# Performance work log

Hardware: AMD Instinct MI355X
Metric: run time of the kernel (lower is better)

## Reference

```python
import jax, jax.numpy as jnp
import numpy as np

D_MODEL = 768
N_CH = 2
D_STATE = 16
RANK = 8
LORA_SCALE = 2.0  # alpha/rank = (rank*2.0)/rank
N_LOOPS = 4       # MAX_INFER_LOOPS
BATCH = 1
SEQ = 1024
EPS = 1e-6        # RMSNorm eps


def setup_inputs() -> dict:
    key = jax.random.key(0)
    ks = jax.random.split(key, 12)
    f32 = jnp.float32
    n = lambda k, shp, s: jax.random.normal(k, shp, dtype=f32) * s
    return {
        "x": jax.random.normal(ks[0], (BATCH, SEQ, D_MODEL), dtype=f32),
        "in_proj_base": n(ks[1], (N_CH * D_MODEL, D_MODEL), 0.02),
        "lora_A": n(ks[2], (RANK, D_MODEL), 0.05),
        "lora_B": n(ks[3], (N_CH * D_MODEL, RANK), 0.05),
        "A_theta": n(ks[4], (N_CH, D_MODEL, D_STATE), 0.1),
        "B_real": n(ks[5], (N_CH, D_MODEL, D_STATE), 0.1),
        "B_imag": n(ks[6], (N_CH, D_MODEL, D_STATE), 0.1),
        "C_real": n(ks[7], (N_CH, D_MODEL, D_STATE), 0.1),
        "C_imag": n(ks[8], (N_CH, D_MODEL, D_STATE), 0.1),
        "out_proj_w": n(ks[9], (D_MODEL, N_CH * D_MODEL), 0.02),
        "mixer_norm_w": jnp.ones((D_MODEL,), f32),
        "loop_norm_w": jnp.ones((D_MODEL,), f32),
        "step_emb": n(ks[10], (N_LOOPS, D_MODEL), 0.02),
    }


def _rmsnorm(v, w):
    return v * jax.lax.rsqrt(jnp.mean(v * v, axis=-1, keepdims=True) + EPS) * w


def reference(x, in_proj_base, lora_A, lora_B, A_theta, B_real, B_imag,
              C_real, C_imag, out_proj_w, mixer_norm_w, loop_norm_w, step_emb):
    Bsz, Lsz, d = x.shape
    # LoRA-merged in_proj weight: base + scale * (B @ A)  [loop-invariant]
    W_in = in_proj_base + LORA_SCALE * (lora_B @ lora_A)  # [2d, d]
    cos_t = jnp.cos(A_theta)[None, None]  # [1,1,ch,d,s]
    sin_t = jnp.sin(A_theta)[None, None]
    Br = B_real[None, None]; Bi = B_imag[None, None]
    Cr = C_real[None, None]; Ci = C_imag[None, None]
    real = jnp.zeros((Bsz, Lsz, N_CH, d, D_STATE), x.dtype)
    imag = jnp.zeros_like(real)
    for i in range(N_LOOPS):  # fixed outer reasoning loop
        h = x + step_emb[i]
        # Mamba3ReasoningBlock: in_proj -> complex rotation state update -> sum over d_state
        x_in = (h @ W_in.T).reshape(Bsz, Lsz, N_CH, d)[..., None]  # [B,L,ch,d,1]
        new_real = cos_t * real - sin_t * imag + Br * x_in
        new_imag = sin_t * real + cos_t * imag + Bi * x_in
        y = (Cr * new_real - Ci * new_imag).sum(-1).reshape(Bsz, Lsz, N_CH * d)
        out = _rmsnorm(y @ out_proj_w.T, mixer_norm_w)
        x = _rmsnorm(h + out, loop_norm_w)  # residual + loop_norm
        real, imag = new_real, new_imag
    return x
```

## Files before the change

kernel.cpp:

```cpp
#include <hip/hip_runtime.h>

#define D_MODEL   768
#define TWO_D     1536
#define SEQ       1024
#define N_LOOPS   4
#define RANK      8
#define D_STATE   16
#define EPS       1e-6f

typedef unsigned short u16;
typedef short s16x8 __attribute__((ext_vector_type(8)));
typedef unsigned short u16x4 __attribute__((ext_vector_type(4)));
typedef float f32x4 __attribute__((ext_vector_type(4)));

#if defined(__has_builtin)
#  if __has_builtin(__builtin_amdgcn_global_load_lds)
#    define HAS_GLL 1
#  endif
#endif
#ifndef HAS_GLL
#  define HAS_GLL 0
#endif

__device__ inline u16 f2bf(float f) {
    union { float f; unsigned u; } v; v.f = f;
    unsigned r = v.u + 0x7fffu + ((v.u >> 16) & 1u);
    return (u16)(r >> 16);
}
__device__ inline float bf2f(u16 b) {
    union { unsigned u; float f; } v; v.u = ((unsigned)b) << 16;
    return v.f;
}

__device__ inline void gll16(const u16* g, u16* l) {
#if HAS_GLL
    __builtin_amdgcn_global_load_lds(
        (__attribute__((address_space(1))) void*)(g),
        (__attribute__((address_space(3))) void*)(l), 16, 0, 0);
#else
    const int ln = threadIdx.x & 63;
    *reinterpret_cast<uint4*>(l + ln * 8) = *reinterpret_cast<const uint4*>(g);
#endif
}

__global__ __launch_bounds__(256) void prep_all(
    const float* __restrict__ base, const float* __restrict__ lA,
    const float* __restrict__ lB,   const float* __restrict__ wout,
    const float* __restrict__ x,    const float* __restrict__ emb0,
    const float* __restrict__ th,   const float* __restrict__ Br,
    const float* __restrict__ Bi,   const float* __restrict__ Cr,
    const float* __restrict__ Ci,
    u16* __restrict__ Wbf, u16* __restrict__ Woutbf, float* __restrict__ G,
    float* __restrict__ hf, u16* __restrict__ hb)
{
    const int b = blockIdx.x, t = threadIdx.x;
    if (b < 1152) {
        int i0 = (b * 256 + t) * 4;
        int r = i0 / D_MODEL, c = i0 % D_MODEL;
        float4 a = *reinterpret_cast<const float4*>(&base[i0]);
#pragma unroll
        for (int k = 0; k < RANK; ++k) {
            float bk = 2.0f * lB[r * RANK + k];
            const float4 av = *reinterpret_cast<const float4*>(&lA[k * D_MODEL + c]);
            a.x += bk * av.x; a.y += bk * av.y; a.z += bk * av.z; a.w += bk * av.w;
        }
        u16x4 o; o.x = f2bf(a.x); o.y = f2bf(a.y); o.z = f2bf(a.z); o.w = f2bf(a.w);
        *reinterpret_cast<u16x4*>(&Wbf[i0]) = o;
    } else if (b < 2304) {
        int i0 = ((b - 1152) * 256 + t) * 4;
        const float4 v = *reinterpret_cast<const float4*>(&wout[i0]);
        u16x4 o; o.x = f2bf(v.x); o.y = f2bf(v.y); o.z = f2bf(v.z); o.w = f2bf(v.w);
        *reinterpret_cast<u16x4*>(&Woutbf[i0]) = o;
    } else if (b < 3072) {
        int i0 = ((b - 2304) * 256 + t) * 4;
        int d = i0 % D_MODEL;
        const float4 v = *reinterpret_cast<const float4*>(&x[i0]);
        const float4 e = *reinterpret_cast<const float4*>(&emb0[d]);
        float4 h = make_float4(v.x + e.x, v.y + e.y, v.z + e.z, v.w + e.w);
        *reinterpret_cast<float4*>(&hf[i0]) = h;
        u16x4 o; o.x = f2bf(h.x); o.y = f2bf(h.y); o.z = f2bf(h.z); o.w = f2bf(h.w);
        *reinterpret_cast<u16x4*>(&hb[i0]) = o;
    } else {
        int cd = (b - 3072) * 256 + t;
        if (cd >= TWO_D) return;
        float g0 = 0.f, g1 = 0.f, g2 = 0.f, g3 = 0.f;
        for (int s = 0; s < D_STATE; ++s) {
            int idx = cd * D_STATE + s;
            float tt = th[idx];
            float br = Br[idx], bi = Bi[idx];
            float cr = Cr[idx], ci = Ci[idx];
#pragma unroll
            for (int k = 0; k < 4; ++k) {
                float ck = cosf(k * tt), sk = sinf(k * tt);
                float er = ck * br - sk * bi;
                float ei = sk * br + ck * bi;
                float g  = cr * er - ci * ei;
                if (k == 0) g0 += g; else if (k == 1) g1 += g;
                else if (k == 2) g2 += g; else g3 += g;
            }
        }
        G[0 * TWO_D + cd] = g0; G[1 * TWO_D + cd] = g1;
        G[2 * TWO_D + cd] = g2; G[3 * TWO_D + cd] = g3;
    }
}

__global__ __launch_bounds__(256) void gemm_nt(
    const u16* __restrict__ A, const int lda,
    const u16* __restrict__ B, const int ldb,
    const int Kz, float* __restrict__ Cp, const int ldc)
{
    __shared__ __align__(16) u16 Al[64 * 64];
    __shared__ __align__(16) u16 Bl[64 * 64];
    const int t = threadIdx.x;
    const int bm = blockIdx.y, bn = blockIdx.x, kz = blockIdx.z;
    const int lane = t & 63, w = t >> 6;
    const int wr = w >> 1, wc = w & 1;
    const int lr = lane & 15, kg = lane >> 4;
    const int kbase = kz * Kz;

    const u16* Aga = A + (size_t)(bm * 64 + w * 16 + (lane >> 3)) * lda + kbase + (lane & 7) * 8;
    const u16* Bga = B + (size_t)(bn * 64 + w * 16 + (lane >> 3)) * ldb + kbase + (lane & 7) * 8;
    u16* Alp = &Al[(w * 16) * 64];
    u16* Blp = &Bl[(w * 16) * 64];

    f32x4 acc[2][2] = {};
    for (int k0 = 0; k0 < Kz; k0 += 64) {
        gll16(Aga + k0, Alp);
        gll16(Aga + (size_t)8 * lda + k0, Alp + 8 * 64);
        gll16(Bga + k0, Blp);
        gll16(Bga + (size_t)8 * ldb + k0, Blp + 8 * 64);
        __syncthreads();
#pragma unroll
        for (int ks = 0; ks < 2; ++ks) {
            const int co = ks * 32 + kg * 8;
            s16x8 a0 = *reinterpret_cast<const s16x8*>(&Al[(wr * 32 +      lr) * 64 + co]);
            s16x8 a1 = *reinterpret_cast<const s16x8*>(&Al[(wr * 32 + 16 + lr) * 64 + co]);
            s16x8 b0 = *reinterpret_cast<const s16x8*>(&Bl[(wc * 32 +      lr) * 64 + co]);
            s16x8 b1 = *reinterpret_cast<const s16x8*>(&Bl[(wc * 32 + 16 + lr) * 64 + co]);
            acc[0][0] = __builtin_amdgcn_mfma_f32_16x16x32_bf16(a0, b0, acc[0][0], 0, 0, 0);
            acc[0][1] = __builtin_amdgcn_mfma_f32_16x16x32_bf16(a0, b1, acc[0][1], 0, 0, 0);
            acc[1][0] = __builtin_amdgcn_mfma_f32_16x16x32_bf16(a1, b0, acc[1][0], 0, 0, 0);
            acc[1][1] = __builtin_amdgcn_mfma_f32_16x16x32_bf16(a1, b1, acc[1][1], 0, 0, 0);
        }
        __syncthreads();
    }
    const int row0 = bm * 64 + wr * 32 + kg * 4;
    const int col0 = bn * 64 + wc * 32 + lr;
    float* Cz = Cp + (size_t)kz * SEQ * ldc;
#pragma unroll
    for (int m = 0; m < 2; ++m)
#pragma unroll
        for (int n = 0; n < 2; ++n)
#pragma unroll
            for (int r = 0; r < 4; ++r)
                Cz[(size_t)(row0 + m * 16 + r) * ldc + col0 + n * 16] = acc[m][n][r];
}

__global__ __launch_bounds__(256) void y_kernel(
    const float* __restrict__ p,
    u16* __restrict__ xin,
    const float* __restrict__ G,
    const int li, u16* __restrict__ y)
{
    int i4 = blockIdx.x * 256 + threadIdx.x;
    int base = i4 * 4;
    int cd = base % TWO_D;
    const float4 v0 = *reinterpret_cast<const float4*>(&p[base]);
    const float4 v1 = *reinterpret_cast<const float4*>(&p[(size_t)SEQ * TWO_D + base]);
    float4 s = make_float4(v0.x + v1.x, v0.y + v1.y, v0.z + v1.z, v0.w + v1.w);
    u16x4 xo; xo.x = f2bf(s.x); xo.y = f2bf(s.y); xo.z = f2bf(s.z); xo.w = f2bf(s.w);
    *reinterpret_cast<u16x4*>(&xin[(size_t)li * SEQ * TWO_D + base]) = xo;
    const float4 g0 = *reinterpret_cast<const float4*>(&G[cd]);
    float s0 = g0.x * s.x, s1 = g0.y * s.y, s2 = g0.z * s.z, s3 = g0.w * s.w;
    for (int j = 0; j < li; ++j) {
        u16x4 v = *reinterpret_cast<const u16x4*>(&xin[(size_t)j * SEQ * TWO_D + base]);
        const float4 g = *reinterpret_cast<const float4*>(&G[(size_t)(li - j) * TWO_D + cd]);
        s0 += bf2f(v.x) * g.x; s1 += bf2f(v.y) * g.y;
        s2 += bf2f(v.z) * g.z; s3 += bf2f(v.w) * g.w;
    }
    u16x4 o; o.x = f2bf(s0); o.y = f2bf(s1); o.z = f2bf(s2); o.w = f2bf(s3);
    *reinterpret_cast<u16x4*>(&y[base]) = o;
}

__global__ __launch_bounds__(256) void norm_kernel(
    const float* __restrict__ q,
    const float* __restrict__ hprev,
    const float* __restrict__ mw,  const float* __restrict__ lw,
    const float* __restrict__ embn,
    float* __restrict__ dstf, u16* __restrict__ dstb)
{
    const int r = blockIdx.x * 4 + (threadIdx.x >> 6);
    const int lane = threadIdx.x & 63;
    const size_t ro = (size_t)r * D_MODEL;
    const size_t PS = (size_t)SEQ * D_MODEL;
    float op[12], h[12];
    float ss = 0.f;
#pragma unroll
    for (int e = 0; e < 12; ++e) {
        int d = lane + e * 64;
        op[e] = (q[ro + d] + q[PS + ro + d]) + (q[2 * PS + ro + d] + q[3 * PS + ro + d]);
        h[e]  = hprev[ro + d];
        ss += op[e] * op[e];
    }
#pragma unroll
    for (int off = 32; off > 0; off >>= 1) ss += __shfl_xor(ss, off, 64);
    const float rs1 = rsqrtf(ss * (1.0f / D_MODEL) + EPS);
    float tt[12];
    float ss2 = 0.f;
#pragma unroll
    for (int e = 0; e < 12; ++e) {
        int d = lane + e * 64;
        tt[e] = h[e] + op[e] * rs1 * mw[d];
        ss2 += tt[e] * tt[e];
    }
#pragma unroll
    for (int off = 32; off > 0; off >>= 1) ss2 += __shfl_xor(ss2, off, 64);
    const float rs2 = rsqrtf(ss2 * (1.0f / D_MODEL) + EPS);
#pragma unroll
    for (int e = 0; e < 12; ++e) {
        int d = lane + e * 64;
        float xo = tt[e] * rs2 * lw[d];
        if (embn != nullptr) {
            float hn = xo + embn[d];
            dstf[ro + d] = hn;
            dstb[ro + d] = f2bf(hn);
        } else {
            dstf[ro + d] = xo;
        }
    }
}

extern "C" void kernel_launch(void* const* d_in, const int* in_sizes, int n_in,
                              void* d_out, int out_size, void* d_ws, size_t ws_size,
                              hipStream_t stream) {
    const float* x            = (const float*)d_in[0];
    const float* in_proj_base = (const float*)d_in[1];
    const float* lora_A       = (const float*)d_in[2];
    const float* lora_B       = (const float*)d_in[3];
    const float* A_theta      = (const float*)d_in[4];
    const float* B_real       = (const float*)d_in[5];
    const float* B_imag       = (const float*)d_in[6];
    const float* C_real       = (const float*)d_in[7];
    const float* C_imag       = (const float*)d_in[8];
    const float* out_proj_w   = (const float*)d_in[9];
    const float* mixer_w      = (const float*)d_in[10];
    const float* loop_w       = (const float*)d_in[11];
    const float* step_emb     = (const float*)d_in[12];
    float* out = (float*)d_out;

    char* p8 = (char*)d_ws;
    u16*   Wbf    = (u16*)p8;   p8 += (size_t)TWO_D * D_MODEL * 2;
    u16*   Woutbf = (u16*)p8;   p8 += (size_t)D_MODEL * TWO_D * 2;
    float* G      = (float*)p8; p8 += (size_t)4 * TWO_D * 4;
    u16*   xin    = (u16*)p8;   p8 += (size_t)N_LOOPS * SEQ * TWO_D * 2;
    u16*   ybf    = (u16*)p8;   p8 += (size_t)SEQ * TWO_D * 2;
    float* hf     = (float*)p8; p8 += (size_t)SEQ * D_MODEL * 4;
    u16*   hbf    = (u16*)p8;   p8 += (size_t)SEQ * D_MODEL * 2;
    float* pbuf   = (float*)p8; p8 += (size_t)2 * SEQ * TWO_D * 4;
    float* qbuf   = (float*)p8; p8 += (size_t)4 * SEQ * D_MODEL * 4;

    prep_all<<<3078, 256, 0, stream>>>(
        in_proj_base, lora_A, lora_B, out_proj_w, x, step_emb,
        A_theta, B_real, B_imag, C_real, C_imag,
        Wbf, Woutbf, G, hf, hbf);

    for (int i = 0; i < N_LOOPS; ++i) {
        const bool last = (i == N_LOOPS - 1);
        gemm_nt<<<dim3(TWO_D / 64, SEQ / 64, 2), 256, 0, stream>>>(
            hbf, D_MODEL, Wbf, D_MODEL, D_MODEL / 2, pbuf, TWO_D);
        y_kernel<<<(SEQ * TWO_D / 4) / 256, 256, 0, stream>>>(pbuf, xin, G, i, ybf);
        gemm_nt<<<dim3(D_MODEL / 64, SEQ / 64, 4), 256, 0, stream>>>(
            ybf, TWO_D, Woutbf, TWO_D, TWO_D / 4, qbuf, D_MODEL);
        norm_kernel<<<SEQ / 4, 256, 0, stream>>>(
            qbuf, hf, mixer_w, loop_w,
            last ? nullptr : (step_emb + (size_t)(i + 1) * D_MODEL),
            last ? out : hf,
            last ? nullptr : hbf);
    }
}
```

Baseline: 234.1 us.

## Double-buffer GEMM LDS tiles, narrow N tile, drop in_proj split-K

The GEMM kernel now double-buffers its LDS tiles so the load of the next K tile is issued before the current tile's MFMAs. Its N tile shrinks from 64 to 32, which keeps the grid large even with less split-K. The in_proj GEMM no longer splits K and writes bf16 directly into the xin history buffer, so the y kernel stops reading and reducing fp32 partial sums. The out_proj split-K drops from 4 to 2, halving the partial-sum traffic read by the norm kernel, at the cost of longer per-block K loops and lower per-block MFMA reuse.

```diff
diff --git a/kernel.cpp b/kernel.cpp
--- a/kernel.cpp
+++ b/kernel.cpp
@@ -104,13 +104,14 @@
     }
 }
 
+template<bool OUT_BF16>
 __global__ __launch_bounds__(256) void gemm_nt(
     const u16* __restrict__ A, const int lda,
     const u16* __restrict__ B, const int ldb,
-    const int Kz, float* __restrict__ Cp, const int ldc)
-{
-    __shared__ __align__(16) u16 Al[64 * 64];
-    __shared__ __align__(16) u16 Bl[64 * 64];
+    const int Kz, void* __restrict__ Cv, const int ldc)
+{
+    __shared__ __align__(16) u16 Al[2][64 * 64];
+    __shared__ __align__(16) u16 Bl[2][32 * 64];
     const int t = threadIdx.x;
     const int bm = blockIdx.y, bn = blockIdx.x, kz = blockIdx.z;
     const int lane = t & 63, w = t >> 6;
@@ -119,62 +120,73 @@
     const int kbase = kz * Kz;
 
     const u16* Aga = A + (size_t)(bm * 64 + w * 16 + (lane >> 3)) * lda + kbase + (lane & 7) * 8;
-    const u16* Bga = B + (size_t)(bn * 64 + w * 16 + (lane >> 3)) * ldb + kbase + (lane & 7) * 8;
-    u16* Alp = &Al[(w * 16) * 64];
-    u16* Blp = &Bl[(w * 16) * 64];
-
-    f32x4 acc[2][2] = {};
-    for (int k0 = 0; k0 < Kz; k0 += 64) {
-        gll16(Aga + k0, Alp);
-        gll16(Aga + (size_t)8 * lda + k0, Alp + 8 * 64);
-        gll16(Bga + k0, Blp);
-        gll16(Bga + (size_t)8 * ldb + k0, Blp + 8 * 64);
-        __syncthreads();
+    const u16* Bga = B + (size_t)(bn * 32 + w * 8  + (lane >> 3)) * ldb + kbase + (lane & 7) * 8;
+
+    f32x4 acc0 = {}, acc1 = {};
+    const int NKT = Kz / 64;
+
+    {
+        u16* Alp = &Al[0][(w * 16) * 64];
+        u16* Blp = &Bl[0][(w * 8) * 64];
+        gll16(Aga, Alp);
+        gll16(Aga + (size_t)8 * lda, Alp + 8 * 64);
+        gll16(Bga, Blp);
+    }
+    __syncthreads();
+
+    for (int kt = 0; kt < NKT; ++kt) {
+        const int cb = kt & 1;
+        if (kt + 1 < NKT) {
+            const int k0 = (kt + 1) * 64;
+            u16* Alp = &Al[cb ^ 1][(w * 16) * 64];
+            u16* Blp = &Bl[cb ^ 1][(w * 8) * 64];
+            gll16(Aga + k0, Alp);
+            gll16(Aga + (size_t)8 * lda + k0, Alp + 8 * 64);
+            gll16(Bga + k0, Blp);
+        }
 #pragma unroll
         for (int ks = 0; ks < 2; ++ks) {
             const int co = ks * 32 + kg * 8;
-            s16x8 a0 = *reinterpret_cast<const s16x8*>(&Al[(wr * 32 +      lr) * 64 + co]);
-            s16x8 a1 = *reinterpret_cast<const s16x8*>(&Al[(wr * 32 + 16 + lr) * 64 + co]);
-            s16x8 b0 = *reinterpret_cast<const s16x8*>(&Bl[(wc * 32 +      lr) * 64 + co]);
-            s16x8 b1 = *reinterpret_cast<const s16x8*>(&Bl[(wc * 32 + 16 + lr) * 64 + co]);
-            acc[0][0] = __builtin_amdgcn_mfma_f32_16x16x32_bf16(a0, b0, acc[0][0], 0, 0, 0);
-            acc[0][1] = __builtin_amdgcn_mfma_f32_16x16x32_bf16(a0, b1, acc[0][1], 0, 0, 0);
-            acc[1][0] = __builtin_amdgcn_mfma_f32_16x16x32_bf16(a1, b0, acc[1][0], 0, 0, 0);
-            acc[1][1] = __builtin_amdgcn_mfma_f32_16x16x32_bf16(a1, b1, acc[1][1], 0, 0, 0);
+            s16x8 a0 = *reinterpret_cast<const s16x8*>(&Al[cb][(wr * 32 +      lr) * 64 + co]);
+            s16x8 a1 = *reinterpret_cast<const s16x8*>(&Al[cb][(wr * 32 + 16 + lr) * 64 + co]);
+            s16x8 b0 = *reinterpret_cast<const s16x8*>(&Bl[cb][(wc * 16 +      lr) * 64 + co]);
+            acc0 = __builtin_amdgcn_mfma_f32_16x16x32_bf16(a0, b0, acc0, 0, 0, 0);
+            acc1 = __builtin_amdgcn_mfma_f32_16x16x32_bf16(a1, b0, acc1, 0, 0, 0);
         }
         __syncthreads();
     }
+
     const int row0 = bm * 64 + wr * 32 + kg * 4;
-    const int col0 = bn * 64 + wc * 32 + lr;
-    float* Cz = Cp + (size_t)kz * SEQ * ldc;
-#pragma unroll
-    for (int m = 0; m < 2; ++m)
-#pragma unroll
-        for (int n = 0; n < 2; ++n)
-#pragma unroll
-            for (int r = 0; r < 4; ++r)
-                Cz[(size_t)(row0 + m * 16 + r) * ldc + col0 + n * 16] = acc[m][n][r];
+    const int col0 = bn * 32 + wc * 16 + lr;
+    if (OUT_BF16) {
+        u16* C = (u16*)Cv;
+#pragma unroll
+        for (int r = 0; r < 4; ++r) {
+            C[(size_t)(row0 + r)      * ldc + col0] = f2bf(acc0[r]);
+            C[(size_t)(row0 + 16 + r) * ldc + col0] = f2bf(acc1[r]);
+        }
+    } else {
+        float* C = (float*)Cv + (size_t)kz * SEQ * ldc;
+#pragma unroll
+        for (int r = 0; r < 4; ++r) {
+            C[(size_t)(row0 + r)      * ldc + col0] = acc0[r];
+            C[(size_t)(row0 + 16 + r) * ldc + col0] = acc1[r];
+        }
+    }
 }
 
 __global__ __launch_bounds__(256) void y_kernel(
-    const float* __restrict__ p,
-    u16* __restrict__ xin,
+    const u16* __restrict__ xin,
     const float* __restrict__ G,
-    const int li, u16* __restrict__ y)
+    const int nacc, u16* __restrict__ y)
 {
     int i4 = blockIdx.x * 256 + threadIdx.x;
     int base = i4 * 4;
     int cd = base % TWO_D;
-    const float4 v0 = *reinterpret_cast<const float4*>(&p[base]);
-    const float4 v1 = *reinterpret_cast<const float4*>(&p[(size_t)SEQ * TWO_D + base]);
-    float4 s = make_float4(v0.x + v1.x, v0.y + v1.y, v0.z + v1.z, v0.w + v1.w);
-    u16x4 xo; xo.x = f2bf(s.x); xo.y = f2bf(s.y); xo.z = f2bf(s.z); xo.w = f2bf(s.w);
-    *reinterpret_cast<u16x4*>(&xin[(size_t)li * SEQ * TWO_D + base]) = xo;
-    const float4 g0 = *reinterpret_cast<const float4*>(&G[cd]);
-    float s0 = g0.x * s.x, s1 = g0.y * s.y, s2 = g0.z * s.z, s3 = g0.w * s.w;
-    for (int j = 0; j < li; ++j) {
+    float s0 = 0.f, s1 = 0.f, s2 = 0.f, s3 = 0.f;
+    for (int j = 0; j < nacc; ++j) {
         u16x4 v = *reinterpret_cast<const u16x4*>(&xin[(size_t)j * SEQ * TWO_D + base]);
-        const float4 g = *reinterpret_cast<const float4*>(&G[(size_t)(li - j) * TWO_D + cd]);
+        const float4 g = *reinterpret_cast<const float4*>(&G[(size_t)(nacc - 1 - j) * TWO_D + cd]);
         s0 += bf2f(v.x) * g.x; s1 += bf2f(v.y) * g.y;
         s2 += bf2f(v.z) * g.z; s3 += bf2f(v.w) * g.w;
     }
@@ -198,7 +210,7 @@
 #pragma unroll
     for (int e = 0; e < 12; ++e) {
         int d = lane + e * 64;
-        op[e] = (q[ro + d] + q[PS + ro + d]) + (q[2 * PS + ro + d] + q[3 * PS + ro + d]);
+        op[e] = q[ro + d] + q[PS + ro + d];
         h[e]  = hprev[ro + d];
         ss += op[e] * op[e];
     }
@@ -256,8 +268,7 @@
     u16*   ybf    = (u16*)p8;   p8 += (size_t)SEQ * TWO_D * 2;
     float* hf     = (float*)p8; p8 += (size_t)SEQ * D_MODEL * 4;
     u16*   hbf    = (u16*)p8;   p8 += (size_t)SEQ * D_MODEL * 2;
-    float* pbuf   = (float*)p8; p8 += (size_t)2 * SEQ * TWO_D * 4;
-    float* qbuf   = (float*)p8; p8 += (size_t)4 * SEQ * D_MODEL * 4;
+    float* qbuf   = (float*)p8; p8 += (size_t)2 * SEQ * D_MODEL * 4;
 
     prep_all<<<3078, 256, 0, stream>>>(
         in_proj_base, lora_A, lora_B, out_proj_w, x, step_emb,
@@ -266,11 +277,12 @@
 
     for (int i = 0; i < N_LOOPS; ++i) {
         const bool last = (i == N_LOOPS - 1);
-        gemm_nt<<<dim3(TWO_D / 64, SEQ / 64, 2), 256, 0, stream>>>(
-            hbf, D_MODEL, Wbf, D_MODEL, D_MODEL / 2, pbuf, TWO_D);
-        y_kernel<<<(SEQ * TWO_D / 4) / 256, 256, 0, stream>>>(pbuf, xin, G, i, ybf);
-        gemm_nt<<<dim3(D_MODEL / 64, SEQ / 64, 4), 256, 0, stream>>>(
-            ybf, TWO_D, Woutbf, TWO_D, TWO_D / 4, qbuf, D_MODEL);
+        gemm_nt<true><<<dim3(TWO_D / 32, SEQ / 64, 1), 256, 0, stream>>>(
+            hbf, D_MODEL, Wbf, D_MODEL, D_MODEL,
+            (void*)(xin + (size_t)i * SEQ * TWO_D), TWO_D);
+        y_kernel<<<(SEQ * TWO_D / 4) / 256, 256, 0, stream>>>(xin, G, i + 1, ybf);
+        gemm_nt<false><<<dim3(D_MODEL / 32, SEQ / 64, 2), 256, 0, stream>>>(
+            ybf, TWO_D, Woutbf, TWO_D, TWO_D / 2, (void*)qbuf, D_MODEL);
         norm_kernel<<<SEQ / 4, 256, 0, stream>>>(
             qbuf, hf, mixer_w, loop_w,
             last ? nullptr : (step_emb + (size_t)(i + 1) * D_MODEL),
```

New measurement: 241.7 us. 3.3% more time.
